# Performance work log

Hardware: AMD Instinct MI355X
Metric: run time of the kernel (lower is better)

Reference implementation:

```python
import jax, jax.numpy as jnp
import numpy as np

DIM = 1280
NUM_HEADS = 16
HEAD_DIM = DIM // NUM_HEADS  # 80
HIDDEN = DIM * 4             # 5120
SEQ = 4096
EPS = 1e-6


def _layernorm(x, scale, bias):
    mu = jnp.mean(x, axis=-1, keepdims=True)
    var = jnp.mean((x - mu) ** 2, axis=-1, keepdims=True)
    return (x - mu) * jax.lax.rsqrt(var + EPS) * scale + bias


def _rotate_half(x):
    x1, x2 = jnp.split(x, 2, axis=-1)
    return jnp.concatenate([-x2, x1], axis=-1)


def _apply_rope(x, freqs):
    # x: [N, H, D], freqs: [N, D//2]
    orig = x.dtype
    x = x.astype(jnp.float32)
    cos = jnp.repeat(jnp.cos(freqs), 2, axis=-1)[:, None, :].astype(jnp.float32)  # [N,1,D]
    sin = jnp.repeat(jnp.sin(freqs), 2, axis=-1)[:, None, :].astype(jnp.float32)
    return (x * cos + _rotate_half(x) * sin).astype(orig)


def _quick_gelu(x):
    return x * jax.nn.sigmoid(1.702 * x)


def setup_inputs() -> dict:
    key = jax.random.key(0)
    ks = jax.random.split(key, 12)
    s = 0.02
    inp = {
        "hidden_states": jax.random.normal(ks[0], (SEQ, DIM), dtype=jnp.float32),
        "rotary_pos_emb": jax.random.normal(ks[1], (SEQ, HEAD_DIM // 2), dtype=jnp.float32),
        "cu_seqlens": jnp.array([0, 1024, 2048, 3072, 4096], dtype=jnp.int32),
        "w_qkv": jax.random.normal(ks[2], (DIM, 3 * DIM), dtype=jnp.float32) * s,
        "b_qkv": jnp.zeros((3 * DIM,), dtype=jnp.float32),
        "w_proj": jax.random.normal(ks[3], (DIM, DIM), dtype=jnp.float32) * s,
        "b_proj": jnp.zeros((DIM,), dtype=jnp.float32),
        "w_fc1": jax.random.normal(ks[4], (DIM, HIDDEN), dtype=jnp.float32) * s,
        "b_fc1": jnp.zeros((HIDDEN,), dtype=jnp.float32),
        "w_fc2": jax.random.normal(ks[5], (HIDDEN, DIM), dtype=jnp.float32) * s,
        "b_fc2": jnp.zeros((DIM,), dtype=jnp.float32),
        "ln1_scale": jnp.ones((DIM,), dtype=jnp.float32),
        "ln1_bias": jnp.zeros((DIM,), dtype=jnp.float32),
        "ln2_scale": jnp.ones((DIM,), dtype=jnp.float32),
        "ln2_bias": jnp.zeros((DIM,), dtype=jnp.float32),
    }
    return inp


def _attention(x, cu_seqlens, rotary_pos_emb, w_qkv, b_qkv, w_proj, b_proj):
    N = x.shape[0]
    qkv = (x @ w_qkv + b_qkv).reshape(N, 3, NUM_HEADS, HEAD_DIM)
    q, k, v = qkv[:, 0], qkv[:, 1], qkv[:, 2]  # each [N, H, D]
    q = _apply_rope(q, rotary_pos_emb)
    k = _apply_rope(k, rotary_pos_emb)
    # block-diagonal mask from cu_seqlens (faithful to original construction)
    row_ids = jnp.arange(N)[None, None, :]
    col_ids = jnp.arange(N)[None, :, None]
    starts = cu_seqlens[:-1][:, None, None]
    ends = cu_seqlens[1:][:, None, None]
    is_valid = (row_ids >= starts) & (row_ids < ends) & (col_ids >= starts) & (col_ids < ends)
    combined = jnp.any(is_valid, axis=0)  # [N, N]
    bias = jnp.where(combined, 0.0, jnp.finfo(q.dtype).min)
    scores = jnp.einsum("shd,thd->hst", q, k) / np.sqrt(HEAD_DIM).astype(np.float32)
    scores = scores + bias[None, :, :]
    probs = jax.nn.softmax(scores.astype(jnp.float32), axis=-1).astype(q.dtype)
    out = jnp.einsum("hst,thd->shd", probs, v).reshape(N, DIM)
    return out @ w_proj + b_proj


def reference(hidden_states, rotary_pos_emb, cu_seqlens, w_qkv, b_qkv, w_proj, b_proj,
              w_fc1, b_fc1, w_fc2, b_fc2, ln1_scale, ln1_bias, ln2_scale, ln2_bias):
    h = hidden_states
    h = h + _attention(_layernorm(h, ln1_scale, ln1_bias), cu_seqlens, rotary_pos_emb,
                       w_qkv, b_qkv, w_proj, b_proj)
    m = _layernorm(h, ln2_scale, ln2_bias)
    h = h + (_quick_gelu(m @ w_fc1 + b_fc1) @ w_fc2 + b_fc2)
    return h
```

## Files before the change

### kernel.cpp

```cpp
#include <hip/hip_runtime.h>
#include <hip/hip_bf16.h>
#include <math.h>

typedef __bf16 bf16;
typedef __bf16 bf16x8 __attribute__((ext_vector_type(8)));
typedef float f32x4 __attribute__((ext_vector_type(4)));

#define DIM 1280
#define SEQ 4096
#define NH 16
#define HD 80
#define HIDDEN 5120
#define FLAG_THRESH 4096

__device__ __forceinline__ void gl_lds16(const bf16* g, bf16* l) {
  __builtin_amdgcn_global_load_lds((const __attribute__((address_space(1))) void*)g,
                                   (__attribute__((address_space(3))) void*)l, 16, 0, 0);
}

__device__ __forceinline__ f32x4 fz4() { f32x4 v; v.x = 0.f; v.y = 0.f; v.z = 0.f; v.w = 0.f; return v; }

__device__ __forceinline__ float ldx(const void* p, size_t i, bool f32) {
  if (f32) return ((const float*)p)[i];
  return (float)((const bf16*)p)[i];
}

__global__ void zero_flag_k(int* flag) { *flag = 0; }

__global__ __launch_bounds__(256) void sniff_k(const unsigned short* h, int n, int* flag) {
  int i = blockIdx.x * 256 + threadIdx.x;
  int c = 0;
  for (int idx = i; idx < n; idx += 256 * gridDim.x) {
    int e = (h[idx] >> 7) & 0xFF;
    c += (e >= 0xC8) ? 1 : 0;
  }
  #pragma unroll
  for (int o = 32; o; o >>= 1) c += __shfl_down(c, o);
  if ((threadIdx.x & 63) == 0 && c) atomicAdd(flag, c);
}

__global__ __launch_bounds__(256) void transpose_k(const void* __restrict__ in, bf16* __restrict__ out,
                                                   int R, int C, const int* __restrict__ flag) {
  bool f32 = *flag > FLAG_THRESH;
  __shared__ bf16 tile[32][33];
  int c0 = blockIdx.x * 32, r0 = blockIdx.y * 32;
  int tx = threadIdx.x, ty = threadIdx.y;
  #pragma unroll
  for (int i = 0; i < 4; i++)
    tile[ty + 8 * i][tx] = (bf16)ldx(in, (size_t)(r0 + ty + 8 * i) * C + c0 + tx, f32);
  __syncthreads();
  #pragma unroll
  for (int i = 0; i < 4; i++)
    out[(size_t)(c0 + ty + 8 * i) * R + r0 + tx] = tile[tx][ty + 8 * i];
}

__global__ __launch_bounds__(256) void ln_k(const void* __restrict__ x, const void* __restrict__ sc,
                                            const void* __restrict__ bi, bf16* __restrict__ out,
                                            const int* __restrict__ flag, int force_f32) {
  bool pf32 = *flag > FLAG_THRESH;
  bool xf32 = force_f32 || pf32;
  int row = blockIdx.x, t = threadIdx.x;
  float v[5];
  float s = 0.f, sq = 0.f;
  #pragma unroll
  for (int i = 0; i < 5; i++) {
    v[i] = ldx(x, (size_t)row * DIM + i * 256 + t, xf32);
    s += v[i]; sq += v[i] * v[i];
  }
  #pragma unroll
  for (int o = 32; o; o >>= 1) { s += __shfl_down(s, o); sq += __shfl_down(sq, o); }
  __shared__ float rs[4], rq[4];
  if ((t & 63) == 0) { rs[t >> 6] = s; rq[t >> 6] = sq; }
  __syncthreads();
  s = rs[0] + rs[1] + rs[2] + rs[3];
  sq = rq[0] + rq[1] + rq[2] + rq[3];
  float mean = s * (1.f / DIM);
  float var = sq * (1.f / DIM) - mean * mean;
  float rstd = rsqrtf(fmaxf(var, 0.f) + 1e-6f);
  #pragma unroll
  for (int i = 0; i < 5; i++) {
    int c = i * 256 + t;
    out[(size_t)row * DIM + c] = (bf16)((v[i] - mean) * rstd * ldx(sc, c, pf32) + ldx(bi, c, pf32));
  }
}

template <int MODE, int NT>
__global__ __launch_bounds__(256) void gemm_bt(const bf16* __restrict__ A, const bf16* __restrict__ Bt,
                                               const void* __restrict__ bias, const void* __restrict__ res,
                                               void* __restrict__ out, int M, int N, int K,
                                               const int* __restrict__ flag) {
  bool pf32 = *flag > FLAG_THRESH;
  constexpr int TN = NT / 32;
  __shared__ bf16 As[128 * 32];
  __shared__ bf16 Bs[NT * 32];
  int tid = threadIdx.x;
  int lane = tid & 63, wv = tid >> 6;
  int quad = lane >> 4, l15 = lane & 15;
  int m0 = blockIdx.y * 128, n0 = blockIdx.x * NT;
  int wm = (wv & 1) * 64, wn = (wv >> 1) * (NT / 2);
  const bf16* Ag = A + (size_t)m0 * K;
  const bf16* Bg = Bt + (size_t)n0 * K;
  int r0 = tid >> 2, c0 = (tid & 3) * 8;
  int r1 = r0 + 64;
  f32x4 acc[4][TN];
  #pragma unroll
  for (int i = 0; i < 4; i++)
    #pragma unroll
    for (int j = 0; j < TN; j++) acc[i][j] = fz4();

  for (int k0 = 0; k0 < K; k0 += 32) {
    gl_lds16(Ag + (size_t)r0 * K + k0 + c0, &As[tid * 8]);
    gl_lds16(Ag + (size_t)r1 * K + k0 + c0, &As[(tid + 256) * 8]);
    gl_lds16(Bg + (size_t)r0 * K + k0 + c0, &Bs[tid * 8]);
    if constexpr (NT == 128) gl_lds16(Bg + (size_t)r1 * K + k0 + c0, &Bs[(tid + 256) * 8]);
    __syncthreads();
    bf16x8 af[4], bfr[TN];
    #pragma unroll
    for (int tm = 0; tm < 4; tm++) af[tm] = *(const bf16x8*)&As[(wm + tm * 16 + l15) * 32 + quad * 8];
    #pragma unroll
    for (int tn = 0; tn < TN; tn++) bfr[tn] = *(const bf16x8*)&Bs[(wn + tn * 16 + l15) * 32 + quad * 8];
    #pragma unroll
    for (int tm = 0; tm < 4; tm++)
      #pragma unroll
      for (int tn = 0; tn < TN; tn++)
        acc[tm][tn] = __builtin_amdgcn_mfma_f32_16x16x32_bf16(af[tm], bfr[tn], acc[tm][tn], 0, 0, 0);
    __syncthreads();
  }

  #pragma unroll
  for (int tm = 0; tm < 4; tm++) {
    #pragma unroll
    for (int tn = 0; tn < TN; tn++) {
      #pragma unroll
      for (int r = 0; r < 4; r++) {
        int row = m0 + wm + tm * 16 + quad * 4 + r;
        int col = n0 + wn + tn * 16 + l15;
        size_t idx = (size_t)row * N + col;
        float vv = acc[tm][tn][r] + ldx(bias, col, pf32);
        if constexpr (MODE == 0) ((bf16*)out)[idx] = (bf16)vv;
        if constexpr (MODE == 1) ((float*)out)[idx] = vv + ldx(res, idx, pf32);
        if constexpr (MODE == 2) ((bf16*)out)[idx] = (bf16)(vv / (1.f + expf(-1.702f * vv)));
      }
    }
  }
}

__global__ __launch_bounds__(256) void gemm_sk(const bf16* __restrict__ A, const bf16* __restrict__ Bt,
                                               float* __restrict__ part, int M, int N, int K, int chunk) {
  __shared__ bf16 As[128 * 32];
  __shared__ bf16 Bs[64 * 32];
  int tid = threadIdx.x;
  int lane = tid & 63, wv = tid >> 6;
  int quad = lane >> 4, l15 = lane & 15;
  int m0 = blockIdx.y * 128, n0 = blockIdx.x * 64;
  int wm = (wv & 1) * 64, wn = (wv >> 1) * 32;
  int kb = blockIdx.z * chunk;
  const bf16* Ag = A + (size_t)m0 * K;
  const bf16* Bg = Bt + (size_t)n0 * K;
  int r0 = tid >> 2, c0 = (tid & 3) * 8;
  int r1 = r0 + 64;
  f32x4 acc[4][2];
  #pragma unroll
  for (int i = 0; i < 4; i++)
    #pragma unroll
    for (int j = 0; j < 2; j++) acc[i][j] = fz4();

  for (int k0 = kb; k0 < kb + chunk; k0 += 32) {
    gl_lds16(Ag + (size_t)r0 * K + k0 + c0, &As[tid * 8]);
    gl_lds16(Ag + (size_t)r1 * K + k0 + c0, &As[(tid + 256) * 8]);
    gl_lds16(Bg + (size_t)r0 * K + k0 + c0, &Bs[tid * 8]);
    __syncthreads();
    bf16x8 af[4], bfr[2];
    #pragma unroll
    for (int tm = 0; tm < 4; tm++) af[tm] = *(const bf16x8*)&As[(wm + tm * 16 + l15) * 32 + quad * 8];
    #pragma unroll
    for (int tn = 0; tn < 2; tn++) bfr[tn] = *(const bf16x8*)&Bs[(wn + tn * 16 + l15) * 32 + quad * 8];
    #pragma unroll
    for (int tm = 0; tm < 4; tm++)
      #pragma unroll
      for (int tn = 0; tn < 2; tn++)
        acc[tm][tn] = __builtin_amdgcn_mfma_f32_16x16x32_bf16(af[tm], bfr[tn], acc[tm][tn], 0, 0, 0);
    __syncthreads();
  }

  float* po = part + (size_t)blockIdx.z * M * N;
  #pragma unroll
  for (int tm = 0; tm < 4; tm++) {
    #pragma unroll
    for (int tn = 0; tn < 2; tn++) {
      #pragma unroll
      for (int r = 0; r < 4; r++) {
        int row = m0 + wm + tm * 16 + quad * 4 + r;
        int col = n0 + wn + tn * 16 + l15;
        po[(size_t)row * N + col] = acc[tm][tn][r];
      }
    }
  }
}

__global__ __launch_bounds__(256) void reduce2_k(const float* __restrict__ p0, const float* __restrict__ p1,
                                                 const void* __restrict__ bias, const float* __restrict__ res,
                                                 float* __restrict__ out, int NCOL,
                                                 const int* __restrict__ flag) {
  bool pf32 = *flag > FLAG_THRESH;
  size_t i = ((size_t)blockIdx.x * 256 + threadIdx.x) * 4;
  int col = (int)(i % NCOL);
  float4 a = *(const float4*)&p0[i];
  float4 b = *(const float4*)&p1[i];
  float4 r = *(const float4*)&res[i];
  float4 o;
  o.x = a.x + b.x + r.x + ldx(bias, col + 0, pf32);
  o.y = a.y + b.y + r.y + ldx(bias, col + 1, pf32);
  o.z = a.z + b.z + r.z + ldx(bias, col + 2, pf32);
  o.w = a.w + b.w + r.w + ldx(bias, col + 3, pf32);
  *(float4*)&out[i] = o;
}

__global__ __launch_bounds__(256) void rope_k(bf16* __restrict__ qkv, const void* __restrict__ rot,
                                              const int* __restrict__ flag) {
  bool pf32 = *flag > FLAG_THRESH;
  int idx = blockIdx.x * 256 + threadIdx.x;
  int d = idx % 40;
  int t = idx / 40;
  int head = t & 15;
  int seq = t >> 4;
  float f1 = ldx(rot, (size_t)seq * 40 + (d >> 1), pf32);
  float f2 = ldx(rot, (size_t)seq * 40 + (d >> 1) + 20, pf32);
  float c1 = cosf(f1), s1 = sinf(f1), c2 = cosf(f2), s2 = sinf(f2);
  const float scq = 0.11180339887498949f;
  size_t base = (size_t)seq * (3 * DIM) + head * HD + d;
  float x1 = (float)qkv[base], x2 = (float)qkv[base + 40];
  qkv[base] = (bf16)((x1 * c1 - x2 * s1) * scq);
  qkv[base + 40] = (bf16)((x2 * c2 + x1 * s2) * scq);
  x1 = (float)qkv[base + DIM]; x2 = (float)qkv[base + DIM + 40];
  qkv[base + DIM] = (bf16)(x1 * c1 - x2 * s1);
  qkv[base + DIM + 40] = (bf16)(x2 * c2 + x1 * s2);
}

__global__ __launch_bounds__(256, 4) void attn_k(const bf16* __restrict__ qkv, const int* __restrict__ cu,
                                                 bf16* __restrict__ out) {
  __shared__ __align__(16) char smem[38144];
  bf16* Qs = (bf16*)smem;
  bf16* Ks = (bf16*)(smem + 13312);
  bf16* Vt = (bf16*)(smem + 26624);
  bf16* Ps = (bf16*)smem;
  int tid = threadIdx.x, lane = tid & 63, wv = tid >> 6;
  int quad = lane >> 4, l15 = lane & 15;
  int qt = blockIdx.x, head = blockIdx.y, seg = blockIdx.z;
  int s0 = cu[seg], s1 = cu[seg + 1];
  int q0 = s0 + qt * 64;
  if (q0 >= s1) return;
  const bf16* qh = qkv + head * HD;
  const bf16* kh = qkv + DIM + head * HD;
  const bf16* vh = qkv + 2 * DIM + head * HD;
  const int RS = 3 * DIM;
  uint4 z4; z4.x = 0; z4.y = 0; z4.z = 0; z4.w = 0;
  for (int i = tid; i < 128; i += 256) {
    int r = i >> 1, c = i & 1;
    *(uint4*)&Qs[r * 104 + 80 + c * 8] = z4;
    *(uint4*)&Ks[r * 104 + 80 + c * 8] = z4;
  }
  for (int i = tid; i < 640; i += 256) {
    int r = i / 10, c = i % 10;
    *(bf16x8*)&Qs[r * 104 + c * 8] = *(const bf16x8*)&qh[(size_t)(q0 + r) * RS + c * 8];
  }
  __syncthreads();
  bf16x8 aq[3];
  #pragma unroll
  for (int ks = 0; ks < 3; ks++)
    aq[ks] = *(const bf16x8*)&Qs[(wv * 16 + l15) * 104 + ks * 32 + quad * 8];

  float m_r[4], l_r[4];
  f32x4 oacc[5];
  #pragma unroll
  for (int r = 0; r < 4; r++) { m_r[r] = -1e30f; l_r[r] = 0.f; }
  #pragma unroll
  for (int nt = 0; nt < 5; nt++) oacc[nt] = fz4();

  for (int kt = s0; kt < s1; kt += 64) {
    __syncthreads();
    for (int i = tid; i < 640; i += 256) {
      int r = i / 10, c = i % 10;
      *(bf16x8*)&Ks[r * 104 + c * 8] = *(const bf16x8*)&kh[(size_t)(kt + r) * RS + c * 8];
    }
    for (int i = tid; i < 640; i += 256) {
      int c = i >> 6, r = i & 63;
      bf16x8 vv = *(const bf16x8*)&vh[(size_t)(kt + r) * RS + c * 8];
      #pragma unroll
      for (int j = 0; j < 8; j++) Vt[(c * 8 + j) * 72 + r] = vv[j];
    }
    __syncthreads();
    f32x4 sacc[4];
    #pragma unroll
    for (int j = 0; j < 4; j++) sacc[j] = fz4();
    #pragma unroll
    for (int ks = 0; ks < 3; ks++) {
      #pragma unroll
      for (int j = 0; j < 4; j++) {
        bf16x8 bk = *(const bf16x8*)&Ks[(j * 16 + l15) * 104 + ks * 32 + quad * 8];
        sacc[j] = __builtin_amdgcn_mfma_f32_16x16x32_bf16(aq[ks], bk, sacc[j], 0, 0, 0);
      }
    }
    #pragma unroll
    for (int r = 0; r < 4; r++) {
      float mx = fmaxf(fmaxf(sacc[0][r], sacc[1][r]), fmaxf(sacc[2][r], sacc[3][r]));
      #pragma unroll
      for (int o = 8; o; o >>= 1) mx = fmaxf(mx, __shfl_xor(mx, o));
      float mnew = fmaxf(m_r[r], mx);
      float alpha = __expf(m_r[r] - mnew);
      float psum = 0.f;
      #pragma unroll
      for (int j = 0; j < 4; j++) {
        float p = __expf(sacc[j][r] - mnew);
        psum += p;
        Ps[wv * 1152 + (quad * 4 + r) * 72 + j * 16 + l15] = (bf16)p;
      }
      #pragma unroll
      for (int o = 8; o; o >>= 1) psum += __shfl_xor(psum, o);
      l_r[r] = l_r[r] * alpha + psum;
      m_r[r] = mnew;
      #pragma unroll
      for (int nt = 0; nt < 5; nt++) oacc[nt][r] *= alpha;
    }
    #pragma unroll
    for (int ks = 0; ks < 2; ks++) {
      bf16x8 ap = *(const bf16x8*)&Ps[wv * 1152 + l15 * 72 + ks * 32 + quad * 8];
      #pragma unroll
      for (int nt = 0; nt < 5; nt++) {
        bf16x8 bv = *(const bf16x8*)&Vt[(nt * 16 + l15) * 72 + ks * 32 + quad * 8];
        oacc[nt] = __builtin_amdgcn_mfma_f32_16x16x32_bf16(ap, bv, oacc[nt], 0, 0, 0);
      }
    }
  }
  #pragma unroll
  for (int nt = 0; nt < 5; nt++) {
    #pragma unroll
    for (int r = 0; r < 4; r++) {
      int row = q0 + wv * 16 + quad * 4 + r;
      int d = nt * 16 + l15;
      out[(size_t)row * DIM + head * HD + d] = (bf16)(oacc[nt][r] / l_r[r]);
    }
  }
}

#define FLAG_OFF 0UL
#define QKVT_OFF 256UL
#define PROJT_OFF 9830656UL
#define FC1T_OFF 13107456UL
#define FC2T_OFF 26214656UL
#define LN_OFF 39321856UL
#define QKV_OFF 49807616UL
#define PART_OFF 49807616UL
#define AO_OFF 81264896UL
#define H1_OFF 91750656UL
#define FC1O_OFF 112722176UL

extern "C" void kernel_launch(void* const* d_in, const int* in_sizes, int n_in,
                              void* d_out, int out_size, void* d_ws, size_t ws_size,
                              hipStream_t stream) {
  const void* hidden = d_in[0];
  const void* rot    = d_in[1];
  const int*  cu     = (const int*)d_in[2];
  const void* w_qkv  = d_in[3];
  const void* b_qkv  = d_in[4];
  const void* w_proj = d_in[5];
  const void* b_proj = d_in[6];
  const void* w_fc1  = d_in[7];
  const void* b_fc1  = d_in[8];
  const void* w_fc2  = d_in[9];
  const void* b_fc2  = d_in[10];
  const void* ln1s   = d_in[11];
  const void* ln1b   = d_in[12];
  const void* ln2s   = d_in[13];
  const void* ln2b   = d_in[14];

  char* ws = (char*)d_ws;
  int* flag   = (int*)(ws + FLAG_OFF);
  bf16* qkvT  = (bf16*)(ws + QKVT_OFF);
  bf16* projT = (bf16*)(ws + PROJT_OFF);
  bf16* fc1T  = (bf16*)(ws + FC1T_OFF);
  bf16* fc2T  = (bf16*)(ws + FC2T_OFF);
  bf16* ln_bf = (bf16*)(ws + LN_OFF);
  bf16* qkv   = (bf16*)(ws + QKV_OFF);
  float* part = (float*)(ws + PART_OFF);
  bf16* ao    = (bf16*)(ws + AO_OFF);
  float* h1   = (float*)(ws + H1_OFF);
  bf16* fc1o  = (bf16*)(ws + FC1O_OFF);

  zero_flag_k<<<1, 1, 0, stream>>>(flag);
  sniff_k<<<256, 256, 0, stream>>>((const unsigned short*)hidden, SEQ * DIM, flag);

  dim3 tb(32, 8);
  transpose_k<<<dim3(120, 40), tb, 0, stream>>>(w_qkv, qkvT, 1280, 3840, flag);
  transpose_k<<<dim3(40, 40), tb, 0, stream>>>(w_proj, projT, 1280, 1280, flag);
  transpose_k<<<dim3(160, 40), tb, 0, stream>>>(w_fc1, fc1T, 1280, 5120, flag);
  transpose_k<<<dim3(40, 160), tb, 0, stream>>>(w_fc2, fc2T, 5120, 1280, flag);

  ln_k<<<SEQ, 256, 0, stream>>>(hidden, ln1s, ln1b, ln_bf, flag, 0);
  gemm_bt<0, 128><<<dim3(30, 32), 256, 0, stream>>>(ln_bf, qkvT, b_qkv, nullptr, qkv, SEQ, 3 * DIM, DIM, flag);
  rope_k<<<10240, 256, 0, stream>>>(qkv, rot, flag);
  attn_k<<<dim3(16, NH, 4), 256, 0, stream>>>(qkv, cu, ao);
  gemm_bt<1, 64><<<dim3(20, 32), 256, 0, stream>>>(ao, projT, b_proj, hidden, h1, SEQ, DIM, DIM, flag);
  ln_k<<<SEQ, 256, 0, stream>>>(h1, ln2s, ln2b, ln_bf, flag, 1);
  gemm_bt<2, 128><<<dim3(40, 32), 256, 0, stream>>>(ln_bf, fc1T, b_fc1, nullptr, fc1o, SEQ, HIDDEN, DIM, flag);
  gemm_sk<<<dim3(20, 32, 2), 256, 0, stream>>>(fc1o, fc2T, part, SEQ, DIM, HIDDEN, HIDDEN / 2);
  reduce2_k<<<SEQ * DIM / 1024, 256, 0, stream>>>(part, part + (size_t)SEQ * DIM, b_fc2, h1,
                                                  (float*)d_out, DIM, flag);
}
```

Before: 667.4 us.

## Double-buffer GEMM LDS tiles and swizzle workgroup order for cache locality

Both GEMM kernels now keep two LDS buffers and issue the global-to-LDS loads for the next K-step before computing on the current one. The goal is to overlap memory latency with MFMA work and drop one barrier per step. Workgroup IDs are also remapped with an 8-way XCD-style swizzle to improve L2 reuse, and the quick-GELU epilogue switches to the fast __expf. The cost is doubled LDS per block, which may lower occupancy. The loop also assumes K and chunk are multiples of 64, and the swizzle assumes the grid size is divisible by 8.

```diff
diff --git a/kernel.cpp b/kernel.cpp
--- a/kernel.cpp
+++ b/kernel.cpp
@@ -84,6 +84,21 @@
   }
 }
 
+template <int TN>
+__device__ __forceinline__ void gemm_step(const bf16* As, const bf16* Bs, f32x4 (&acc)[4][TN],
+                                          int wm, int wn, int quad, int l15) {
+  bf16x8 af[4], bfr[TN];
+  #pragma unroll
+  for (int tm = 0; tm < 4; tm++) af[tm] = *(const bf16x8*)&As[(wm + tm * 16 + l15) * 32 + quad * 8];
+  #pragma unroll
+  for (int tn = 0; tn < TN; tn++) bfr[tn] = *(const bf16x8*)&Bs[(wn + tn * 16 + l15) * 32 + quad * 8];
+  #pragma unroll
+  for (int tm = 0; tm < 4; tm++)
+    #pragma unroll
+    for (int tn = 0; tn < TN; tn++)
+      acc[tm][tn] = __builtin_amdgcn_mfma_f32_16x16x32_bf16(af[tm], bfr[tn], acc[tm][tn], 0, 0, 0);
+}
+
 template <int MODE, int NT>
 __global__ __launch_bounds__(256) void gemm_bt(const bf16* __restrict__ A, const bf16* __restrict__ Bt,
                                                const void* __restrict__ bias, const void* __restrict__ res,
@@ -91,12 +106,18 @@
                                                const int* __restrict__ flag) {
   bool pf32 = *flag > FLAG_THRESH;
   constexpr int TN = NT / 32;
-  __shared__ bf16 As[128 * 32];
-  __shared__ bf16 Bs[NT * 32];
+  __shared__ bf16 As0[128 * 32];
+  __shared__ bf16 As1[128 * 32];
+  __shared__ bf16 Bs0[NT * 32];
+  __shared__ bf16 Bs1[NT * 32];
   int tid = threadIdx.x;
   int lane = tid & 63, wv = tid >> 6;
   int quad = lane >> 4, l15 = lane & 15;
-  int m0 = blockIdx.y * 128, n0 = blockIdx.x * NT;
+  int nwg = gridDim.x * gridDim.y;
+  int bid = blockIdx.y * gridDim.x + blockIdx.x;
+  int sbid = (bid & 7) * (nwg >> 3) + (bid >> 3);
+  int bx = sbid % gridDim.x, by = sbid / gridDim.x;
+  int m0 = by * 128, n0 = bx * NT;
   int wm = (wv & 1) * 64, wn = (wv >> 1) * (NT / 2);
   const bf16* Ag = A + (size_t)m0 * K;
   const bf16* Bg = Bt + (size_t)n0 * K;
@@ -108,24 +129,24 @@
     #pragma unroll
     for (int j = 0; j < TN; j++) acc[i][j] = fz4();
 
-  for (int k0 = 0; k0 < K; k0 += 32) {
-    gl_lds16(Ag + (size_t)r0 * K + k0 + c0, &As[tid * 8]);
-    gl_lds16(Ag + (size_t)r1 * K + k0 + c0, &As[(tid + 256) * 8]);
-    gl_lds16(Bg + (size_t)r0 * K + k0 + c0, &Bs[tid * 8]);
-    if constexpr (NT == 128) gl_lds16(Bg + (size_t)r1 * K + k0 + c0, &Bs[(tid + 256) * 8]);
-    __syncthreads();
-    bf16x8 af[4], bfr[TN];
-    #pragma unroll
-    for (int tm = 0; tm < 4; tm++) af[tm] = *(const bf16x8*)&As[(wm + tm * 16 + l15) * 32 + quad * 8];
-    #pragma unroll
-    for (int tn = 0; tn < TN; tn++) bfr[tn] = *(const bf16x8*)&Bs[(wn + tn * 16 + l15) * 32 + quad * 8];
-    #pragma unroll
-    for (int tm = 0; tm < 4; tm++)
-      #pragma unroll
-      for (int tn = 0; tn < TN; tn++)
-        acc[tm][tn] = __builtin_amdgcn_mfma_f32_16x16x32_bf16(af[tm], bfr[tn], acc[tm][tn], 0, 0, 0);
-    __syncthreads();
-  }
+#define STAGE_BT(as, bs, kk) do {                                        \
+    gl_lds16(Ag + (size_t)r0 * K + (kk) + c0, &(as)[tid * 8]);           \
+    gl_lds16(Ag + (size_t)r1 * K + (kk) + c0, &(as)[(tid + 256) * 8]);   \
+    gl_lds16(Bg + (size_t)r0 * K + (kk) + c0, &(bs)[tid * 8]);           \
+    if constexpr (NT == 128) gl_lds16(Bg + (size_t)r1 * K + (kk) + c0, &(bs)[(tid + 256) * 8]); \
+  } while (0)
+
+  STAGE_BT(As0, Bs0, 0);
+  __syncthreads();
+  for (int k0 = 0; k0 < K; k0 += 64) {
+    STAGE_BT(As1, Bs1, k0 + 32);
+    gemm_step<TN>(As0, Bs0, acc, wm, wn, quad, l15);
+    __syncthreads();
+    if (k0 + 64 < K) STAGE_BT(As0, Bs0, k0 + 64);
+    gemm_step<TN>(As1, Bs1, acc, wm, wn, quad, l15);
+    __syncthreads();
+  }
+#undef STAGE_BT
 
   #pragma unroll
   for (int tm = 0; tm < 4; tm++) {
@@ -139,7 +160,7 @@
         float vv = acc[tm][tn][r] + ldx(bias, col, pf32);
         if constexpr (MODE == 0) ((bf16*)out)[idx] = (bf16)vv;
         if constexpr (MODE == 1) ((float*)out)[idx] = vv + ldx(res, idx, pf32);
-        if constexpr (MODE == 2) ((bf16*)out)[idx] = (bf16)(vv / (1.f + expf(-1.702f * vv)));
+        if constexpr (MODE == 2) ((bf16*)out)[idx] = (bf16)(vv / (1.f + __expf(-1.702f * vv)));
       }
     }
   }
@@ -147,12 +168,18 @@
 
 __global__ __launch_bounds__(256) void gemm_sk(const bf16* __restrict__ A, const bf16* __restrict__ Bt,
                                                float* __restrict__ part, int M, int N, int K, int chunk) {
-  __shared__ bf16 As[128 * 32];
-  __shared__ bf16 Bs[64 * 32];
+  __shared__ bf16 As0[128 * 32];
+  __shared__ bf16 As1[128 * 32];
+  __shared__ bf16 Bs0[64 * 32];
+  __shared__ bf16 Bs1[64 * 32];
   int tid = threadIdx.x;
   int lane = tid & 63, wv = tid >> 6;
   int quad = lane >> 4, l15 = lane & 15;
-  int m0 = blockIdx.y * 128, n0 = blockIdx.x * 64;
+  int nwg = gridDim.x * gridDim.y;
+  int bid = blockIdx.y * gridDim.x + blockIdx.x;
+  int sbid = (bid & 7) * (nwg >> 3) + (bid >> 3);
+  int bx = sbid % gridDim.x, by = sbid / gridDim.x;
+  int m0 = by * 128, n0 = bx * 64;
   int wm = (wv & 1) * 64, wn = (wv >> 1) * 32;
   int kb = blockIdx.z * chunk;
   const bf16* Ag = A + (size_t)m0 * K;
@@ -165,23 +192,23 @@
     #pragma unroll
     for (int j = 0; j < 2; j++) acc[i][j] = fz4();
 
-  for (int k0 = kb; k0 < kb + chunk; k0 += 32) {
-    gl_lds16(Ag + (size_t)r0 * K + k0 + c0, &As[tid * 8]);
-    gl_lds16(Ag + (size_t)r1 * K + k0 + c0, &As[(tid + 256) * 8]);
-    gl_lds16(Bg + (size_t)r0 * K + k0 + c0, &Bs[tid * 8]);
-    __syncthreads();
-    bf16x8 af[4], bfr[2];
-    #pragma unroll
-    for (int tm = 0; tm < 4; tm++) af[tm] = *(const bf16x8*)&As[(wm + tm * 16 + l15) * 32 + quad * 8];
-    #pragma unroll
-    for (int tn = 0; tn < 2; tn++) bfr[tn] = *(const bf16x8*)&Bs[(wn + tn * 16 + l15) * 32 + quad * 8];
-    #pragma unroll
-    for (int tm = 0; tm < 4; tm++)
-      #pragma unroll
-      for (int tn = 0; tn < 2; tn++)
-        acc[tm][tn] = __builtin_amdgcn_mfma_f32_16x16x32_bf16(af[tm], bfr[tn], acc[tm][tn], 0, 0, 0);
-    __syncthreads();
-  }
+#define STAGE_SK(as, bs, kk) do {                                        \
+    gl_lds16(Ag + (size_t)r0 * K + (kk) + c0, &(as)[tid * 8]);           \
+    gl_lds16(Ag + (size_t)r1 * K + (kk) + c0, &(as)[(tid + 256) * 8]);   \
+    gl_lds16(Bg + (size_t)r0 * K + (kk) + c0, &(bs)[tid * 8]);           \
+  } while (0)
+
+  STAGE_SK(As0, Bs0, kb);
+  __syncthreads();
+  for (int k0 = kb; k0 < kb + chunk; k0 += 64) {
+    STAGE_SK(As1, Bs1, k0 + 32);
+    gemm_step<2>(As0, Bs0, acc, wm, wn, quad, l15);
+    __syncthreads();
+    if (k0 + 64 < kb + chunk) STAGE_SK(As0, Bs0, k0 + 64);
+    gemm_step<2>(As1, Bs1, acc, wm, wn, quad, l15);
+    __syncthreads();
+  }
+#undef STAGE_SK
 
   float* po = part + (size_t)blockIdx.z * M * N;
   #pragma unroll
```

After: 663.9 us. No clear change (-0.5%).
